# Performance work log

Hardware: AMD Instinct MI355X
Metric: run time of the kernel (lower is better)

The kernel has to match this reference:

```python
import jax, jax.numpy as jnp
import numpy as np

B, H, W, C = 8, 64, 64, 512
DQK = C // 8  # query/key channel dim from Conv2D(filters//8, 1)


def setup_inputs() -> dict:
    key = jax.random.key(0)
    ks = jax.random.split(key, 8)
    s_in = 1.0 / np.sqrt(C)
    x = jax.random.normal(ks[0], (B, H, W, C), dtype=jnp.float32)
    Wq = jax.random.normal(ks[1], (C, DQK), dtype=jnp.float32) * s_in
    bq = jnp.zeros((DQK,), dtype=jnp.float32)
    Wk = jax.random.normal(ks[2], (C, DQK), dtype=jnp.float32) * s_in
    bk = jnp.zeros((DQK,), dtype=jnp.float32)
    Wv = jax.random.normal(ks[3], (C, C), dtype=jnp.float32) * s_in
    bv = jnp.zeros((C,), dtype=jnp.float32)
    # gamma initialized to zeros in the original, but use a nonzero value so
    # the attention branch actually contributes to the output/gradients.
    gamma = jnp.ones((1,), dtype=jnp.float32) * 0.5
    return {"x": x, "Wq": Wq, "bq": bq, "Wk": Wk, "bk": bk,
            "Wv": Wv, "bv": bv, "gamma": gamma}


def reference(x, Wq, bq, Wk, bk, Wv, bv, gamma):
    b, h, w, c = x.shape
    n = h * w  # spatial_size
    xf = x.reshape(b, n, c)
    # 1x1 convs == per-pixel channel matmuls
    q = xf @ Wq + bq            # [B, N, C//8]
    k = xf @ Wk + bk            # [B, N, C//8]
    v = xf @ Wv + bv            # [B, N, C]
    # Dot(axes=-1): attn[b,i,j] = sum_d q[b,i,d] * k[b,j,d]
    attn = jnp.einsum('bid,bjd->bij', q, k)
    attn = jax.nn.softmax(attn, axis=-1)
    # Dot(axes=-2): out[b,j,c] = sum_i attn[b,i,j] * v[b,i,c]  (note transpose)
    out = jnp.einsum('bij,bic->bjc', attn, v)
    out = out.reshape(b, h, w, c)
    return gamma * out + x
```

## Files before the change

kernel.cpp:

```cpp
#include <hip/hip_runtime.h>
#include <hip/hip_bf16.h>
#include <cstdio>

typedef unsigned short u16;
typedef __attribute__((ext_vector_type(4))) float f32x4;
typedef __attribute__((ext_vector_type(8))) short s16x8;

__device__ __forceinline__ u16 bf16b(float f) {
  union { float f; unsigned u; } c; c.f = f;
  unsigned u = c.u;
  return (u16)((u + 0x7FFFu + ((u >> 16) & 1u)) >> 16);
}

__device__ __forceinline__ void load16(const void* g, void* l) {
  __builtin_amdgcn_global_load_lds(
      (const __attribute__((address_space(1))) void*)g,
      (__attribute__((address_space(3))) void*)l, 16, 0, 0);
}


__global__ __launch_bounds__(256) void cvt_all_k(const float* __restrict__ x,
                                                 const float* __restrict__ Wq,
                                                 const float* __restrict__ Wk,
                                                 const float* __restrict__ Wv,
                                                 u16* __restrict__ xb,
                                                 u16* __restrict__ Wcat) {
  int bid = blockIdx.x;
  if (bid < 16384) {
    long i = ((long)bid * 256 + threadIdx.x) * 4;
    float4 f = *(const float4*)&x[i];
    unsigned lo = (unsigned)bf16b(f.x) | ((unsigned)bf16b(f.y) << 16);
    unsigned hi = (unsigned)bf16b(f.z) | ((unsigned)bf16b(f.w) << 16);
    uint2 v; v.x = lo; v.y = hi;
    *(uint2*)&xb[i] = v;
  } else {
    int idx = (bid - 16384) * 256 + threadIdx.x;
    int nn = idx >> 9, k = idx & 511;
    float v;
    if (nn < 64)       v = Wq[k * 64 + nn];
    else if (nn < 128) v = Wk[k * 64 + (nn - 64)];
    else               v = Wv[k * 512 + (nn - 128)];
    Wcat[idx] = bf16b(v);
  }
}

__global__ __launch_bounds__(256, 2) void projGemm(
    const u16* __restrict__ A, const u16* __restrict__ B,
    u16* __restrict__ Qb, u16* __restrict__ Kb, u16* __restrict__ Vt,
    const float* __restrict__ bq, const float* __restrict__ bk,
    const float* __restrict__ bv) {
  constexpr int BM = 128, BN = 128, FM = 4, FN = 4;
  __shared__ __align__(16) u16 At[BM * 64];
  __shared__ __align__(16) u16 Bt[BN * 64];
  const int tid = threadIdx.x;
  const int lane = tid & 63, w = tid >> 6;
  const int wr = w >> 1, wc = w & 1;
  const int l15 = lane & 15, lhi = lane >> 4;
  const long m0 = (long)blockIdx.x * BM;
  const long n0 = (long)blockIdx.y * BN;

  f32x4 acc[FM][FN] = {};

  for (int k0 = 0; k0 < 512; k0 += 64) {
#pragma unroll
    for (int it = 0; it < 8; ++it) {
      int q = it * 256 + tid;
      if (q < BM * 8) {
        int row = q >> 3, c8 = q & 7;
        load16(A + (m0 + row) * 512 + k0 + c8 * 8, &At[q * 8]);
      } else {
        int q2 = q - BM * 8;
        int row = q2 >> 3, c8 = q2 & 7;
        load16(B + (n0 + row) * 512 + k0 + c8 * 8, &Bt[q2 * 8]);
      }
    }
    __syncthreads();
#pragma unroll
    for (int kk = 0; kk < 64; kk += 32) {
      s16x8 af[FM], bf[FN];
#pragma unroll
      for (int i = 0; i < FM; ++i)
        af[i] = *(const s16x8*)&At[(wr * 64 + i * 16 + l15) * 64 + kk + lhi * 8];
#pragma unroll
      for (int j = 0; j < FN; ++j)
        bf[j] = *(const s16x8*)&Bt[(wc * 64 + j * 16 + l15) * 64 + kk + lhi * 8];
#pragma unroll
      for (int i = 0; i < FM; ++i)
#pragma unroll
        for (int j = 0; j < FN; ++j)
          acc[i][j] = __builtin_amdgcn_mfma_f32_16x16x32_bf16(af[i], bf[j],
                                                              acc[i][j], 0, 0, 0);
    }
    __syncthreads();
  }

#pragma unroll
  for (int i = 0; i < FM; ++i) {
#pragma unroll
    for (int j = 0; j < FN; ++j) {
      long mm = m0 + wr * 64 + i * 16 + lhi * 4;
      long nn = n0 + wc * 64 + j * 16 + l15;
      if (nn < 64) {
        float bb = bq[nn];
#pragma unroll
        for (int r = 0; r < 4; ++r)
          Qb[(mm + r) * 64 + nn] = bf16b(acc[i][j][r] + bb);
      } else if (nn < 128) {
        float bb = bk[nn - 64];
#pragma unroll
        for (int r = 0; r < 4; ++r)
          Kb[(mm + r) * 64 + nn - 64] = bf16b(acc[i][j][r] + bb);
      } else {
        long c = nn - 128;
        float bb = bv[c];
        unsigned u01 = (unsigned)bf16b(acc[i][j][0] + bb) |
                       ((unsigned)bf16b(acc[i][j][1] + bb) << 16);
        unsigned u23 = (unsigned)bf16b(acc[i][j][2] + bb) |
                       ((unsigned)bf16b(acc[i][j][3] + bb) << 16);
        uint2 u; u.x = u01; u.y = u23;
        *(uint2*)&Vt[(mm >> 12) * 512 * 4096 + c * 4096 + (mm & 4095)] = u;
      }
    }
  }
}

__global__ __launch_bounds__(256, 2) void stats_k(const u16* __restrict__ Qb,
                                                  const u16* __restrict__ Kb,
                                                  float* __restrict__ m_part,
                                                  float* __restrict__ l_part) {
  const int b = blockIdx.z, jc = blockIdx.y;
  const long i0 = (long)blockIdx.x * 128;
  const u16* Q = Qb + (long)b * 4096 * 64;
  const u16* Kp = Kb + (long)b * 4096 * 64;
  __shared__ __align__(16) u16 Qt[128 * 64];
  __shared__ __align__(16) u16 Kt[128 * 64];
  const int tid = threadIdx.x, lane = tid & 63, w = tid >> 6;
  const int l15 = lane & 15, lhi = lane >> 4;

#pragma unroll
  for (int it = 0; it < 4; ++it) {
    int q = it * 256 + tid;
    int row = q >> 3, c8 = q & 7;
    load16(Q + (i0 + row) * 64 + c8 * 8, &Qt[q * 8]);
  }

  float mrun[2][4], lrun[2][4];
#pragma unroll
  for (int i = 0; i < 2; ++i)
#pragma unroll
    for (int r = 0; r < 4; ++r) { mrun[i][r] = -1e30f; lrun[i][r] = 0.f; }

  for (int jt = 0; jt < 8; ++jt) {
    long j0 = (long)jc * 1024 + jt * 128;
#pragma unroll
    for (int it = 0; it < 4; ++it) {
      int q = it * 256 + tid;
      int row = q >> 3, c8 = q & 7;
      load16(Kp + (j0 + row) * 64 + c8 * 8, &Kt[q * 8]);
    }
    __syncthreads();
    f32x4 acc[2][8] = {};
#pragma unroll
    for (int kk = 0; kk < 64; kk += 32) {
      s16x8 af[2], bf[8];
#pragma unroll
      for (int i = 0; i < 2; ++i)
        af[i] = *(const s16x8*)&Qt[(w * 32 + i * 16 + l15) * 64 + kk + lhi * 8];
#pragma unroll
      for (int j = 0; j < 8; ++j)
        bf[j] = *(const s16x8*)&Kt[(j * 16 + l15) * 64 + kk + lhi * 8];
#pragma unroll
      for (int i = 0; i < 2; ++i)
#pragma unroll
        for (int j = 0; j < 8; ++j)
          acc[i][j] = __builtin_amdgcn_mfma_f32_16x16x32_bf16(af[i], bf[j],
                                                              acc[i][j], 0, 0, 0);
    }
#pragma unroll
    for (int i = 0; i < 2; ++i)
#pragma unroll
      for (int r = 0; r < 4; ++r) {
        float tm = acc[i][0][r];
#pragma unroll
        for (int j = 1; j < 8; ++j) tm = fmaxf(tm, acc[i][j][r]);
        float mo = mrun[i][r];
        float mn = fmaxf(mo, tm);
        float s = 0.f;
#pragma unroll
        for (int j = 0; j < 8; ++j) s += __expf(acc[i][j][r] - mn);
        lrun[i][r] = lrun[i][r] * __expf(mo - mn) + s;
        mrun[i][r] = mn;
      }
    __syncthreads();
  }

#pragma unroll
  for (int i = 0; i < 2; ++i)
#pragma unroll
    for (int r = 0; r < 4; ++r) {
      float m = mrun[i][r], l = lrun[i][r];
#pragma unroll
      for (int d = 1; d < 16; d <<= 1) {
        float mo = __shfl_xor(m, d);
        float lo = __shfl_xor(l, d);
        float mn = fmaxf(m, mo);
        l = l * __expf(m - mn) + lo * __expf(mo - mn);
        m = mn;
      }
      if (l15 == 0) {
        long ig = i0 + w * 32 + i * 16 + lhi * 4 + r;
        long idx = ((long)(b * 4 + jc)) * 4096 + ig;
        m_part[idx] = m;
        l_part[idx] = l;
      }
    }
}

__global__ __launch_bounds__(256) void merge_k(const float* __restrict__ m_part,
                                               const float* __restrict__ l_part,
                                               float* __restrict__ mfin,
                                               float* __restrict__ linv) {
  int idx = blockIdx.x * 256 + threadIdx.x;
  int b = idx >> 12, i = idx & 4095;
  float m = -1e30f, l = 0.f;
#pragma unroll
  for (int jc = 0; jc < 4; ++jc) {
    long o = ((long)(b * 4 + jc)) * 4096 + i;
    float mp = m_part[o], lp = l_part[o];
    float mn = fmaxf(m, mp);
    l = l * __expf(m - mn) + lp * __expf(mp - mn);
    m = mn;
  }
  mfin[idx] = m;
  linv[idx] = 1.0f / l;
}

__global__ __launch_bounds__(256, 2) void fusedPV(
    const u16* __restrict__ Qb, const u16* __restrict__ Kb,
    const u16* __restrict__ Vt, const float* __restrict__ mfin,
    const float* __restrict__ lnv, const float* __restrict__ x,
    const float* __restrict__ gamma, float* __restrict__ out) {
  __shared__ __align__(16) u16 Qc[64 * 64];
  __shared__ __align__(16) u16 Vc[256 * 64];
  __shared__ __align__(16) u16 Pl[128 * 64];
  const int tid = threadIdx.x, lane = tid & 63, w = tid >> 6;
  const int l15 = lane & 15, lhi = lane >> 4;
  const int wi = w & 1, wj = w >> 1, wc = w & 1;
  const int s = blockIdx.x + 32 * (blockIdx.y + 2 * blockIdx.z);
  const int pi = (s & 7) * 64 + (s >> 3);
  const int b = pi >> 6;
  const long c0 = (long)((pi >> 5) & 1) * 256;
  const long j0 = (long)(pi & 31) * 128;
  const u16* Qg = Qb + (long)b * 4096 * 64;
  const u16* Kg = Kb + (long)b * 4096 * 64;
  const u16* Vg = Vt + (long)b * 512 * 4096;
  const float* mg = mfin + (long)b * 4096;
  const float* lg = lnv + (long)b * 4096;
  const float gma = gamma[0];

#pragma unroll
  for (int p = 0; p < 4; ++p) {
    int q = p * 256 + tid;
    int r = q >> 3, col = q & 7, cg = col ^ (r & 7);
    load16(Kg + (j0 + r) * 64 + cg * 8, (char*)Pl + r * 128 + col * 16);
  }
  asm volatile("s_waitcnt vmcnt(0) lgkmcnt(0)\n\ts_barrier" ::: "memory");
  s16x8 kf[4][2];
#pragma unroll
  for (int fj = 0; fj < 4; ++fj)
#pragma unroll
    for (int kx = 0; kx < 2; ++kx) {
      int r = wj * 64 + fj * 16 + l15;
      kf[fj][kx] = *(const s16x8*)((const char*)Pl + r * 128 +
                                   (((kx * 32 + lhi * 8) * 2) ^ ((r & 7) << 4)));
    }
  __syncthreads();

  f32x4 acc2[4][8] = {};

  for (int t = 0; t < 64; ++t) {
    const int i_base = t * 64;
#pragma unroll
    for (int p = 0; p < 2; ++p) {
      int q = p * 256 + tid;
      int r = q >> 3, col = q & 7, cg = col ^ (r & 7);
      load16(Qg + (long)(i_base + r) * 64 + cg * 8,
             (char*)Qc + r * 128 + col * 16);
    }
#pragma unroll
    for (int p = 0; p < 8; ++p) {
      int q = p * 256 + tid;
      int r = q >> 3, col = q & 7, cg = col ^ (r & 7);
      load16(Vg + (c0 + r) * 4096 + i_base + cg * 8,
             (char*)Vc + r * 128 + col * 16);
    }
    __syncthreads();

    f32x4 acc1[2][4] = {};
#pragma unroll
    for (int kx = 0; kx < 2; ++kx) {
      s16x8 af[2];
#pragma unroll
      for (int fi = 0; fi < 2; ++fi) {
        int r = wi * 32 + fi * 16 + l15;
        af[fi] = *(const s16x8*)((const char*)Qc + r * 128 +
                                 (((kx * 32 + lhi * 8) * 2) ^ ((r & 7) << 4)));
      }
#pragma unroll
      for (int fi = 0; fi < 2; ++fi)
#pragma unroll
        for (int fj = 0; fj < 4; ++fj)
          acc1[fi][fj] = __builtin_amdgcn_mfma_f32_16x16x32_bf16(
              af[fi], kf[fj][kx], acc1[fi][fj], 0, 0, 0);
    }

#pragma unroll
    for (int fi = 0; fi < 2; ++fi) {
      int i0l = wi * 32 + fi * 16 + lhi * 4;
      f32x4 mv = *(const f32x4*)&mg[i_base + i0l];
      f32x4 lv = *(const f32x4*)&lg[i_base + i0l];
#pragma unroll
      for (int fj = 0; fj < 4; ++fj) {
        int j = wj * 64 + fj * 16 + l15;
        float p0 = __expf(acc1[fi][fj][0] - mv[0]) * lv[0];
        float p1 = __expf(acc1[fi][fj][1] - mv[1]) * lv[1];
        float p2 = __expf(acc1[fi][fj][2] - mv[2]) * lv[2];
        float p3 = __expf(acc1[fi][fj][3] - mv[3]) * lv[3];
        uint2 u;
        u.x = (unsigned)bf16b(p0) | ((unsigned)bf16b(p1) << 16);
        u.y = (unsigned)bf16b(p2) | ((unsigned)bf16b(p3) << 16);
        *(uint2*)((char*)Pl + j * 128 + ((i0l * 2) ^ ((j & 7) << 4))) = u;
      }
    }
    __syncthreads();

    __builtin_amdgcn_s_setprio(1);
#pragma unroll
    for (int kx = 0; kx < 2; ++kx) {
      int kk = kx * 32;
      s16x8 pa[4];
#pragma unroll
      for (int fm = 0; fm < 4; ++fm) {
        int r = wj * 64 + fm * 16 + l15;
        pa[fm] = *(const s16x8*)((const char*)Pl + r * 128 +
                                 (((kk + lhi * 8) * 2) ^ ((r & 7) << 4)));
      }
#pragma unroll
      for (int fn = 0; fn < 8; ++fn) {
        int r = wc * 128 + fn * 16 + l15;
        s16x8 vb = *(const s16x8*)((const char*)Vc + r * 128 +
                                   (((kk + lhi * 8) * 2) ^ ((r & 7) << 4)));
#pragma unroll
        for (int fm = 0; fm < 4; ++fm)
          acc2[fm][fn] = __builtin_amdgcn_mfma_f32_16x16x32_bf16(
              pa[fm], vb, acc2[fm][fn], 0, 0, 0);
      }
    }
    __builtin_amdgcn_s_setprio(0);
    __syncthreads();
  }

#pragma unroll
  for (int fm = 0; fm < 4; ++fm) {
#pragma unroll
    for (int fn = 0; fn < 8; ++fn) {
      long j = j0 + wj * 64 + fm * 16 + lhi * 4;
      long c = c0 + wc * 128 + fn * 16 + l15;
#pragma unroll
      for (int r = 0; r < 4; ++r) {
        long o = ((long)b * 4096 + j + r) * 512 + c;
        out[o] = gma * acc2[fm][fn][r] + x[o];
      }
    }
  }
}


extern "C" void kernel_launch(void* const* d_in, const int* in_sizes, int n_in,
                              void* d_out, int out_size, void* d_ws,
                              size_t ws_size, hipStream_t stream) {
  const float* x = (const float*)d_in[0];
  const float* Wq = (const float*)d_in[1];
  const float* bq = (const float*)d_in[2];
  const float* Wk = (const float*)d_in[3];
  const float* bk = (const float*)d_in[4];
  const float* Wv = (const float*)d_in[5];
  const float* bv = (const float*)d_in[6];
  const float* gamma = (const float*)d_in[7];
  float* out = (float*)d_out;

  char* ws = (char*)d_ws;
  size_t off = 0;
  auto alloc = [&](size_t bytes) {
    char* p = ws + off;
    off += (bytes + 255) & ~(size_t)255;
    return p;
  };
  u16* xb = (u16*)alloc((size_t)32768 * 512 * 2);
  u16* Wcat = (u16*)alloc((size_t)640 * 512 * 2);
  u16* Qb = (u16*)alloc((size_t)8 * 4096 * 64 * 2);
  u16* Kb = (u16*)alloc((size_t)8 * 4096 * 64 * 2);
  u16* Vt = (u16*)alloc((size_t)8 * 512 * 4096 * 2);
  float* m_part = (float*)alloc((size_t)8 * 4 * 4096 * 4);
  float* l_part = (float*)alloc((size_t)8 * 4 * 4096 * 4);
  float* mfin = (float*)alloc((size_t)8 * 4096 * 4);
  float* lnv = (float*)alloc((size_t)8 * 4096 * 4);
  if (off > ws_size) {
    fprintf(stderr, "kernel_launch: ws too small: need %zu have %zu\n", off,
            ws_size);
    return;
  }

  cvt_all_k<<<16384 + 1280, 256, 0, stream>>>(x, Wq, Wk, Wv, xb, Wcat);
  projGemm<<<dim3(256, 5, 1), 256, 0, stream>>>(xb, Wcat, Qb, Kb, Vt, bq, bk,
                                                bv);
  stats_k<<<dim3(32, 4, 8), 256, 0, stream>>>(Qb, Kb, m_part, l_part);
  merge_k<<<128, 256, 0, stream>>>(m_part, l_part, mfin, lnv);
  fusedPV<<<dim3(32, 2, 8), 256, 0, stream>>>(Qb, Kb, Vt, mfin, lnv, x,
                                              gamma, out);
}
```

Measured before the change: 304.6 us.

## Load Q and V fragments directly to registers, fold softmax normalizer into exp2

The fusedPV kernel no longer stages Q and V tiles through LDS. Each wave loads its MFMA operand fragments straight from global memory into registers. The work split changes so each wave owns 64 output channels across all 128 j rows, and one barrier per iteration is dropped. The merge kernel now emits m*log2e + log2(l), so P is computed with a single exp2 and no reciprocal multiply, and the separate linv buffer is removed. The risk is uncoalesced or unhidden global latency, since the V row loads are strided by 4096 elements, and higher register pressure from the 8x4 accumulator plus the register-held V.

```diff
diff --git a/kernel.cpp b/kernel.cpp
--- a/kernel.cpp
+++ b/kernel.cpp
@@ -5,6 +5,8 @@
 typedef unsigned short u16;
 typedef __attribute__((ext_vector_type(4))) float f32x4;
 typedef __attribute__((ext_vector_type(8))) short s16x8;
+
+#define LOG2E 1.4426950408889634f
 
 __device__ __forceinline__ u16 bf16b(float f) {
   union { float f; unsigned u; } c; c.f = f;
@@ -218,8 +220,7 @@
 
 __global__ __launch_bounds__(256) void merge_k(const float* __restrict__ m_part,
                                                const float* __restrict__ l_part,
-                                               float* __restrict__ mfin,
-                                               float* __restrict__ linv) {
+                                               float* __restrict__ mfin) {
   int idx = blockIdx.x * 256 + threadIdx.x;
   int b = idx >> 12, i = idx & 4095;
   float m = -1e30f, l = 0.f;
@@ -231,21 +232,18 @@
     l = l * __expf(m - mn) + lp * __expf(mp - mn);
     m = mn;
   }
-  mfin[idx] = m;
-  linv[idx] = 1.0f / l;
+  mfin[idx] = fmaf(m, LOG2E, __log2f(l));
 }
 
 __global__ __launch_bounds__(256, 2) void fusedPV(
     const u16* __restrict__ Qb, const u16* __restrict__ Kb,
     const u16* __restrict__ Vt, const float* __restrict__ mfin,
-    const float* __restrict__ lnv, const float* __restrict__ x,
-    const float* __restrict__ gamma, float* __restrict__ out) {
-  __shared__ __align__(16) u16 Qc[64 * 64];
-  __shared__ __align__(16) u16 Vc[256 * 64];
+    const float* __restrict__ x, const float* __restrict__ gamma,
+    float* __restrict__ out) {
   __shared__ __align__(16) u16 Pl[128 * 64];
   const int tid = threadIdx.x, lane = tid & 63, w = tid >> 6;
   const int l15 = lane & 15, lhi = lane >> 4;
-  const int wi = w & 1, wj = w >> 1, wc = w & 1;
+  const int wi = w & 1, wj = w >> 1;
   const int s = blockIdx.x + 32 * (blockIdx.y + 2 * blockIdx.z);
   const int pi = (s & 7) * 64 + (s >> 3);
   const int b = pi >> 6;
@@ -255,7 +253,6 @@
   const u16* Kg = Kb + (long)b * 4096 * 64;
   const u16* Vg = Vt + (long)b * 512 * 4096;
   const float* mg = mfin + (long)b * 4096;
-  const float* lg = lnv + (long)b * 4096;
   const float gma = gamma[0];
 
 #pragma unroll
@@ -276,96 +273,76 @@
     }
   __syncthreads();
 
-  f32x4 acc2[4][8] = {};
+  f32x4 acc2[8][4] = {};
 
   for (int t = 0; t < 64; ++t) {
     const int i_base = t * 64;
-#pragma unroll
-    for (int p = 0; p < 2; ++p) {
-      int q = p * 256 + tid;
-      int r = q >> 3, col = q & 7, cg = col ^ (r & 7);
-      load16(Qg + (long)(i_base + r) * 64 + cg * 8,
-             (char*)Qc + r * 128 + col * 16);
-    }
-#pragma unroll
-    for (int p = 0; p < 8; ++p) {
-      int q = p * 256 + tid;
-      int r = q >> 3, col = q & 7, cg = col ^ (r & 7);
-      load16(Vg + (c0 + r) * 4096 + i_base + cg * 8,
-             (char*)Vc + r * 128 + col * 16);
-    }
-    __syncthreads();
-
-    f32x4 acc1[2][4] = {};
-#pragma unroll
-    for (int kx = 0; kx < 2; ++kx) {
-      s16x8 af[2];
-#pragma unroll
-      for (int fi = 0; fi < 2; ++fi) {
-        int r = wi * 32 + fi * 16 + l15;
-        af[fi] = *(const s16x8*)((const char*)Qc + r * 128 +
-                                 (((kx * 32 + lhi * 8) * 2) ^ ((r & 7) << 4)));
-      }
-#pragma unroll
-      for (int fi = 0; fi < 2; ++fi)
+    s16x8 qf[2][2], vr[4][2];
+#pragma unroll
+    for (int fi = 0; fi < 2; ++fi)
+#pragma unroll
+      for (int kx = 0; kx < 2; ++kx)
+        qf[fi][kx] = *(const s16x8*)&Qg[(long)(i_base + wi * 32 + fi * 16 +
+                                               l15) * 64 + kx * 32 + lhi * 8];
+#pragma unroll
+    for (int fn = 0; fn < 4; ++fn)
+#pragma unroll
+      for (int kx = 0; kx < 2; ++kx)
+        vr[fn][kx] = *(const s16x8*)&Vg[(c0 + w * 64 + fn * 16 + l15) * 4096 +
+                                        i_base + kx * 32 + lhi * 8];
+    asm volatile("s_waitcnt lgkmcnt(0)\n\ts_barrier" ::: "memory");
+#pragma unroll
+    for (int fi = 0; fi < 2; ++fi) {
+      f32x4 a1[4] = {};
+#pragma unroll
+      for (int kx = 0; kx < 2; ++kx)
 #pragma unroll
         for (int fj = 0; fj < 4; ++fj)
-          acc1[fi][fj] = __builtin_amdgcn_mfma_f32_16x16x32_bf16(
-              af[fi], kf[fj][kx], acc1[fi][fj], 0, 0, 0);
-    }
-
-#pragma unroll
-    for (int fi = 0; fi < 2; ++fi) {
-      int i0l = wi * 32 + fi * 16 + lhi * 4;
+          a1[fj] = __builtin_amdgcn_mfma_f32_16x16x32_bf16(qf[fi][kx],
+                                                           kf[fj][kx], a1[fj],
+                                                           0, 0, 0);
+      const int i0l = wi * 32 + fi * 16 + lhi * 4;
       f32x4 mv = *(const f32x4*)&mg[i_base + i0l];
-      f32x4 lv = *(const f32x4*)&lg[i_base + i0l];
 #pragma unroll
       for (int fj = 0; fj < 4; ++fj) {
         int j = wj * 64 + fj * 16 + l15;
-        float p0 = __expf(acc1[fi][fj][0] - mv[0]) * lv[0];
-        float p1 = __expf(acc1[fi][fj][1] - mv[1]) * lv[1];
-        float p2 = __expf(acc1[fi][fj][2] - mv[2]) * lv[2];
-        float p3 = __expf(acc1[fi][fj][3] - mv[3]) * lv[3];
+        float p0 = __builtin_amdgcn_exp2f(fmaf(a1[fj][0], LOG2E, -mv[0]));
+        float p1 = __builtin_amdgcn_exp2f(fmaf(a1[fj][1], LOG2E, -mv[1]));
+        float p2 = __builtin_amdgcn_exp2f(fmaf(a1[fj][2], LOG2E, -mv[2]));
+        float p3 = __builtin_amdgcn_exp2f(fmaf(a1[fj][3], LOG2E, -mv[3]));
         uint2 u;
         u.x = (unsigned)bf16b(p0) | ((unsigned)bf16b(p1) << 16);
         u.y = (unsigned)bf16b(p2) | ((unsigned)bf16b(p3) << 16);
         *(uint2*)((char*)Pl + j * 128 + ((i0l * 2) ^ ((j & 7) << 4))) = u;
       }
     }
-    __syncthreads();
-
+    asm volatile("s_waitcnt lgkmcnt(0)\n\ts_barrier" ::: "memory");
     __builtin_amdgcn_s_setprio(1);
 #pragma unroll
     for (int kx = 0; kx < 2; ++kx) {
-      int kk = kx * 32;
-      s16x8 pa[4];
-#pragma unroll
-      for (int fm = 0; fm < 4; ++fm) {
-        int r = wj * 64 + fm * 16 + l15;
+      s16x8 pa[8];
+#pragma unroll
+      for (int fm = 0; fm < 8; ++fm) {
+        int r = fm * 16 + l15;
         pa[fm] = *(const s16x8*)((const char*)Pl + r * 128 +
-                                 (((kk + lhi * 8) * 2) ^ ((r & 7) << 4)));
-      }
-#pragma unroll
-      for (int fn = 0; fn < 8; ++fn) {
-        int r = wc * 128 + fn * 16 + l15;
-        s16x8 vb = *(const s16x8*)((const char*)Vc + r * 128 +
-                                   (((kk + lhi * 8) * 2) ^ ((r & 7) << 4)));
-#pragma unroll
-        for (int fm = 0; fm < 4; ++fm)
+                                 (((kx * 32 + lhi * 8) * 2) ^ ((r & 7) << 4)));
+      }
+#pragma unroll
+      for (int fn = 0; fn < 4; ++fn)
+#pragma unroll
+        for (int fm = 0; fm < 8; ++fm)
           acc2[fm][fn] = __builtin_amdgcn_mfma_f32_16x16x32_bf16(
-              pa[fm], vb, acc2[fm][fn], 0, 0, 0);
-      }
+              pa[fm], vr[fn][kx], acc2[fm][fn], 0, 0, 0);
     }
     __builtin_amdgcn_s_setprio(0);
-    __syncthreads();
-  }
-
-#pragma unroll
-  for (int fm = 0; fm < 4; ++fm) {
-#pragma unroll
-    for (int fn = 0; fn < 8; ++fn) {
-      long j = j0 + wj * 64 + fm * 16 + lhi * 4;
-      long c = c0 + wc * 128 + fn * 16 + l15;
+  }
+
+#pragma unroll
+  for (int fm = 0; fm < 8; ++fm) {
+#pragma unroll
+    for (int fn = 0; fn < 4; ++fn) {
+      long j = j0 + fm * 16 + lhi * 4;
+      long c = c0 + w * 64 + fn * 16 + l15;
 #pragma unroll
       for (int r = 0; r < 4; ++r) {
         long o = ((long)b * 4096 + j + r) * 512 + c;
@@ -404,7 +381,6 @@
   float* m_part = (float*)alloc((size_t)8 * 4 * 4096 * 4);
   float* l_part = (float*)alloc((size_t)8 * 4 * 4096 * 4);
   float* mfin = (float*)alloc((size_t)8 * 4096 * 4);
-  float* lnv = (float*)alloc((size_t)8 * 4096 * 4);
   if (off > ws_size) {
     fprintf(stderr, "kernel_launch: ws too small: need %zu have %zu\n", off,
             ws_size);
@@ -415,7 +391,7 @@
   projGemm<<<dim3(256, 5, 1), 256, 0, stream>>>(xb, Wcat, Qb, Kb, Vt, bq, bk,
                                                 bv);
   stats_k<<<dim3(32, 4, 8), 256, 0, stream>>>(Qb, Kb, m_part, l_part);
-  merge_k<<<128, 256, 0, stream>>>(m_part, l_part, mfin, lnv);
-  fusedPV<<<dim3(32, 2, 8), 256, 0, stream>>>(Qb, Kb, Vt, mfin, lnv, x,
-                                              gamma, out);
-}
+  merge_k<<<128, 256, 0, stream>>>(m_part, l_part, mfin);
+  fusedPV<<<dim3(32, 2, 8), 256, 0, stream>>>(Qb, Kb, Vt, mfin, x, gamma,
+                                              out);
+}
```

Result: slower. 389.5 us (+27.9%).
